# Kernel tuning notes

Hardware: AMD Instinct MI355X
Metric: run time of the kernel (lower is better)

The kernel has to match this reference:

```python
import jax, jax.numpy as jnp
import numpy as np

NZ, NC = 100, 2
FEAT_NUMBER, FEATURE_DIM = 8192, 1024
B = 8192
BN_EPS = 1e-5
GUMBEL_EPS = 0.001
TEMP = 0.1


def _batchnorm(h, gamma, beta):
    # torch BatchNorm1d training mode: biased batch statistics
    mu = jnp.mean(h, axis=0, keepdims=True)
    var = jnp.var(h, axis=0, keepdims=True)
    return (h - mu) * jax.lax.rsqrt(var + BN_EPS) * gamma + beta


def setup_inputs() -> dict:
    key = jax.random.key(0)
    ks = jax.random.split(key, 16)
    def glorot(k, shape):
        lim = 1.0 / np.sqrt(shape[0])
        return jax.random.uniform(k, shape, jnp.float32, -lim, lim)
    return {
        "x": jax.random.normal(ks[0], (B, NZ), jnp.float32),
        "y": jax.random.uniform(ks[1], (B, NC), jnp.float32),
        "W1": glorot(ks[2], (NZ + NC, 256)), "b1": jnp.zeros((256,), jnp.float32),
        "g1": jnp.ones((256,), jnp.float32), "be1": jnp.zeros((256,), jnp.float32),
        "W2": glorot(ks[3], (256, 64)), "b2": jnp.zeros((64,), jnp.float32),
        "g2": jnp.ones((64,), jnp.float32), "be2": jnp.zeros((64,), jnp.float32),
        "W3": glorot(ks[4], (64, FEAT_NUMBER)), "b3": jnp.zeros((FEAT_NUMBER,), jnp.float32),
        "codebook": jax.random.normal(ks[5], (FEAT_NUMBER, FEATURE_DIM), jnp.float32),
    }


def reference(x, y, W1, b1, g1, be1, W2, b2, g2, be2, W3, b3, codebook):
    z = jnp.concatenate([x, y], axis=-1)                       # [B, nz+nc]
    h = jax.nn.relu(_batchnorm(z @ W1 + b1, g1, be1))          # [B, 256]
    h = jax.nn.relu(_batchnorm(h @ W2 + b2, g2, be2))          # [B, 64]
    logits = h @ W3 + b3                                       # [B, feat_number]

    # gumbel noise: U = eps*rand; g = -log(-log(U+eps)+eps)
    U = GUMBEL_EPS * jax.random.uniform(jax.random.key(42), logits.shape, jnp.float32)
    g = -jnp.log(-jnp.log(U + GUMBEL_EPS) + GUMBEL_EPS)
    y_soft = jax.nn.softmax((logits + g) / TEMP, axis=-1)

    # straight-through one-hot
    ind = jnp.argmax(y_soft, axis=-1)
    y_hard = jax.nn.one_hot(ind, FEAT_NUMBER, dtype=y_soft.dtype)
    z_st = jax.lax.stop_gradient(y_hard - y_soft) + y_soft     # [B, feat_number]

    # weighted codebook sum == matmul (avoids [B,F,D] broadcast intermediate)
    return jnp.einsum('bf,fd->bd', z_st, codebook)             # [B, feature_dim]
```

## Files before the change

### kernel.cpp

```cpp
#include <hip/hip_runtime.h>
#include <math.h>

#define B_ROWS   8192
#define NZ       100
#define NC       2
#define H1       256
#define H2       64
#define FEATN    8192
#define FDIM     1024
#define RROWS    16
#define NTILE    (FEATN / 16)
#define NTILE_H  (NTILE / 2)
#define A1ROWS   16
#define A1BLKS   (B_ROWS / A1ROWS)
#define CONVBLKS 128
#define A2ROWS   16
#define A2BLKS   (B_ROWS / A2ROWS)

typedef __attribute__((ext_vector_type(8))) short short8;
typedef __attribute__((ext_vector_type(4))) float f32x4;

__device__ __forceinline__ unsigned rotl32(unsigned v, int r) {
    return (v << r) | (v >> (32 - r));
}
__device__ __forceinline__ unsigned threefry_bits(unsigned lo) {
    const unsigned ks0 = 0u, ks1 = 42u, ks2 = 0x1BD11BDAu ^ 42u;
    unsigned x0 = 0u + ks0;
    unsigned x1 = lo + ks1;
#define TF_R4(a,b,c,d) \
    x0 += x1; x1 = rotl32(x1,a); x1 ^= x0; \
    x0 += x1; x1 = rotl32(x1,b); x1 ^= x0; \
    x0 += x1; x1 = rotl32(x1,c); x1 ^= x0; \
    x0 += x1; x1 = rotl32(x1,d); x1 ^= x0;
    TF_R4(13,15,26,6);  x0 += ks1; x1 += ks2 + 1u;
    TF_R4(17,29,16,24); x0 += ks2; x1 += ks0 + 2u;
    TF_R4(13,15,26,6);  x0 += ks0; x1 += ks1 + 3u;
    TF_R4(17,29,16,24); x0 += ks1; x1 += ks2 + 4u;
    TF_R4(13,15,26,6);  x0 += ks2; x1 += ks0 + 5u;
#undef TF_R4
    return x0 ^ x1;
}
__device__ __forceinline__ float gumbel_g(unsigned flat) {
    unsigned bits = threefry_bits(flat);
    float u  = __uint_as_float((bits >> 9) | 0x3f800000u) - 1.0f;
    float U  = 0.001f * u;
    float t1 = U + 0.001f;
    float L1 = (float)log((double)t1);
    float A  = 0.001f - L1;
    float L2 = (float)log((double)A);
    return -L2;
}

__device__ __forceinline__ unsigned short f2bf(float x) {
    unsigned u = __float_as_uint(x);
    u += 0x7fffu + ((u >> 16) & 1u);
    return (unsigned short)(u >> 16);
}
__device__ __forceinline__ unsigned short f2bf_up(float x) {
    unsigned u = __float_as_uint(x);
    unsigned hi = (u & 0x80000000u) ? (u >> 16) : ((u + 0xFFFFu) >> 16);
    return (unsigned short)hi;
}
__device__ __forceinline__ float bf2f(unsigned short h) {
    return __uint_as_float((unsigned)h << 16);
}
__device__ __forceinline__ unsigned fmono(float x) {
    unsigned b = __float_as_uint(x);
    return (b & 0x80000000u) ? ~b : (b | 0x80000000u);
}

__global__ __launch_bounds__(512) void k_a1(
    const float* __restrict__ x, const float* __restrict__ y,
    const float* __restrict__ W1, const float* __restrict__ b1,
    const float* __restrict__ W3,
    float* __restrict__ a1, double* __restrict__ p1, double* __restrict__ p2,
    unsigned short* __restrict__ w3s, float* __restrict__ maxw)
{
    const int t = threadIdx.x;

    if (blockIdx.x >= A1BLKS) {
        const int job  = (blockIdx.x - A1BLKS) * 512 + t;
        const int T    = job >> 7;
        const int rem  = job & 127;
        const int kh   = rem >> 6;
        const int l    = rem & 63;
        const int quad = l >> 4, col = l & 15;
        const float* src = W3 + (size_t)(kh * 32 + quad * 8) * FEATN + T * 16 + col;
        unsigned short v[8];
        float mx = 0.0f;
#pragma unroll
        for (int jj = 0; jj < 8; ++jj) {
            float xv = src[(size_t)jj * FEATN];
            mx = fmaxf(mx, fabsf(xv));
            v[jj] = f2bf(xv);
        }
        uint4 o;
        o.x = (unsigned)v[0] | ((unsigned)v[1] << 16);
        o.y = (unsigned)v[2] | ((unsigned)v[3] << 16);
        o.z = (unsigned)v[4] | ((unsigned)v[5] << 16);
        o.w = (unsigned)v[6] | ((unsigned)v[7] << 16);
        ((uint4*)w3s)[job] = o;
#pragma unroll
        for (int off = 32; off; off >>= 1) mx = fmaxf(mx, __shfl_xor(mx, off));
        __shared__ float wred[8];
        if ((t & 63) == 0) wred[t >> 6] = mx;
        __syncthreads();
        if (t == 0) {
            float m = wred[0];
#pragma unroll
            for (int wq = 1; wq < 8; ++wq) m = fmaxf(m, wred[wq]);
            atomicMax((unsigned*)maxw, __float_as_uint(m));
        }
        return;
    }

    const int j    = t & 255;
    const int half = t >> 8;
    const int b0   = blockIdx.x * A1ROWS;
    const int r0   = half * 8;

    __shared__ __align__(16) float xs[NZ][16];
    __shared__ __align__(16) float ys[NC][16];
    __shared__ float vsh[256][8];
    for (int q = t; q < A1ROWS * NZ; q += 512) {
        int r = q / NZ, i = q - r * NZ;
        xs[i][r] = x[(size_t)b0 * NZ + q];
    }
    if (t < A1ROWS * NC) {
        int r = t >> 1, i = t & 1;
        ys[i][r] = y[b0 * NC + t];
    }
    __syncthreads();

    double acc[8];
#pragma unroll
    for (int r = 0; r < 8; ++r) acc[r] = 0.0;
    for (int i = 0; i < NZ; ++i) {
        double wd = (double)W1[i * H1 + j];
        const float4 x0 = *(const float4*)&xs[i][r0];
        const float4 x1 = *(const float4*)&xs[i][r0 + 4];
        acc[0] += (double)x0.x * wd; acc[1] += (double)x0.y * wd;
        acc[2] += (double)x0.z * wd; acc[3] += (double)x0.w * wd;
        acc[4] += (double)x1.x * wd; acc[5] += (double)x1.y * wd;
        acc[6] += (double)x1.z * wd; acc[7] += (double)x1.w * wd;
    }
#pragma unroll
    for (int i = 0; i < NC; ++i) {
        double wd = (double)W1[(NZ + i) * H1 + j];
        const float4 y0 = *(const float4*)&ys[i][r0];
        const float4 y1 = *(const float4*)&ys[i][r0 + 4];
        acc[0] += (double)y0.x * wd; acc[1] += (double)y0.y * wd;
        acc[2] += (double)y0.z * wd; acc[3] += (double)y0.w * wd;
        acc[4] += (double)y1.x * wd; acc[5] += (double)y1.y * wd;
        acc[6] += (double)y1.z * wd; acc[7] += (double)y1.w * wd;
    }
    const double bb = (double)b1[j];
    float v[8];
#pragma unroll
    for (int r = 0; r < 8; ++r) {
        v[r] = (float)(acc[r] + bb);
        a1[(b0 + r0 + r) * H1 + j] = v[r];
    }
    if (half) {
#pragma unroll
        for (int r = 0; r < 8; ++r) vsh[j][r] = v[r];
    }
    __syncthreads();
    if (!half) {
        double s = 0.0, s2 = 0.0;
#pragma unroll
        for (int r = 0; r < 8; ++r) {
            double dv = (double)v[r];
            s += dv; s2 += dv * dv;
        }
#pragma unroll
        for (int r = 0; r < 8; ++r) {
            double dv = (double)vsh[j][r];
            s += dv; s2 += dv * dv;
        }
        p1[blockIdx.x * H1 + j] = s;
        p2[blockIdx.x * H1 + j] = s2;
    }
}

__global__ __launch_bounds__(256) void k_stats2(
    const double* __restrict__ p1, const double* __restrict__ p2,
    int nprt, int ncol,
    const float* __restrict__ gamma, const float* __restrict__ beta,
    float* __restrict__ scale, float* __restrict__ shift)
{
    const int j = blockIdx.x, t = threadIdx.x;
    double s = 0.0, s2 = 0.0;
    for (int g = t; g < nprt; g += 256) {
        s  += p1[(size_t)g * ncol + j];
        s2 += p2[(size_t)g * ncol + j];
    }
#pragma unroll
    for (int off = 32; off; off >>= 1) {
        s  += __shfl_xor(s, off);
        s2 += __shfl_xor(s2, off);
    }
    __shared__ double ws1[4], ws2[4];
    if ((t & 63) == 0) { ws1[t >> 6] = s; ws2[t >> 6] = s2; }
    __syncthreads();
    if (t == 0) {
        s  = (ws1[0] + ws1[1]) + (ws1[2] + ws1[3]);
        s2 = (ws2[0] + ws2[1]) + (ws2[2] + ws2[3]);
        double mean = s * (1.0 / B_ROWS);
        double var  = s2 * (1.0 / B_ROWS) - mean * mean;
        double rstd = 1.0 / sqrt(var + 1e-5);
        double sc   = (double)gamma[j] * rstd;
        scale[j] = (float)sc;
        shift[j] = (float)((double)beta[j] - mean * sc);
    }
}

__global__ __launch_bounds__(512) void k_a2(
    const float* __restrict__ a1,
    const float* __restrict__ sc1, const float* __restrict__ sh1,
    const float* __restrict__ W2, const float* __restrict__ b2,
    float* __restrict__ a2, double* __restrict__ p1, double* __restrict__ p2)
{
    const int t  = threadIdx.x;
    const int k  = t & 63;
    const int rg = t >> 6;
    const int b0 = blockIdx.x * A2ROWS;
    const int r0 = rg * 2;

    __shared__ __align__(8) float hs[H1][18];
    __shared__ float vsh[64][17];

    {
        const int jc = t & 255, rq = t >> 8;
        const float sct = sc1[jc], sht = sh1[jc];
#pragma unroll
        for (int rr = rq * 8; rr < rq * 8 + 8; ++rr) {
            float vv = a1[(size_t)(b0 + rr) * H1 + jc];
            hs[jc][rr] = fmaxf(fmaf(vv, sct, sht), 0.0f);
        }
    }
    __syncthreads();

    double acc0 = 0.0, acc1 = 0.0;
#pragma unroll 4
    for (int j = 0; j < H1; ++j) {
        double wd = (double)W2[j * H2 + k];
        const float2 h2 = *(const float2*)&hs[j][r0];
        acc0 += (double)h2.x * wd;
        acc1 += (double)h2.y * wd;
    }
    const double bb = (double)b2[k];
    float v0 = (float)(acc0 + bb);
    float v1 = (float)(acc1 + bb);
    a2[(b0 + r0 + 0) * H2 + k] = v0;
    a2[(b0 + r0 + 1) * H2 + k] = v1;
    vsh[k][r0]     = v0;
    vsh[k][r0 + 1] = v1;
    __syncthreads();
    if (t < 64) {
        double s = 0.0, s2 = 0.0;
#pragma unroll
        for (int r = 0; r < A2ROWS; ++r) {
            double dv = (double)vsh[t][r];
            s += dv; s2 += dv * dv;
        }
        p1[blockIdx.x * H2 + t] = s;
        p2[blockIdx.x * H2 + t] = s2;
    }
}

__global__ __launch_bounds__(512)
__attribute__((amdgpu_waves_per_eu(4, 4)))
void k_main(
    const float* __restrict__ a2,
    const float* __restrict__ sc2, const float* __restrict__ sh2,
    const float* __restrict__ W3, const float* __restrict__ b3,
    const unsigned short* __restrict__ w3s, const float* __restrict__ maxw,
    unsigned long long* __restrict__ bestG)
{
    const int t    = threadIdx.x;
    const int wv   = t >> 6;
    const int lane = t & 63;
    const int quad = lane >> 4, col = lane & 15;
    const int half = blockIdx.x & 1;
    const int b0   = (blockIdx.x >> 1) * RROWS;

    __shared__ __align__(16) float h2T[64][17];
    __shared__ unsigned short fineW[NTILE_H][17];
    __shared__ float thrS[RROWS];
    __shared__ unsigned short wl[RROWS * NTILE_H];
    __shared__ int wlN;
    __shared__ float maxwS;

    if (t == 0) { maxwS = maxw[0]; wlN = 0; }
    for (int q = t; q < RROWS * 64; q += 512) {
        int j = q >> 4, r = q & 15;
        float v = a2[(b0 + r) * H2 + j];
        h2T[j][r] = fmaxf(fmaf(v, sc2[j], sh2[j]), 0.0f);
    }
    __syncthreads();

    short8 aF0, aF1;
#pragma unroll
    for (int jj = 0; jj < 8; ++jj) {
        aF0[jj] = (short)f2bf(h2T[quad * 8 + jj][col]);
        aF1[jj] = (short)f2bf(h2T[32 + quad * 8 + jj][col]);
    }

    {
        const uint4*  wp = (const uint4*)w3s
                         + (size_t)(half * NTILE_H + wv * 32) * 128 + lane;
        const float4* bq = (const float4*)b3 + (half * 1024 + wv * 128) + quad;
        for (int s = 0; s < 4; ++s) {
            uint4 c[8], d[8];
            float4 bb[8];
#pragma unroll
            for (int u = 0; u < 8; ++u) {
                c[u]  = wp[u * 128];
                d[u]  = wp[u * 128 + 64];
                bb[u] = bq[u * 4];
            }
#pragma unroll
            for (int u = 0; u < 8; ++u) {
                f32x4 acc = {bb[u].x, bb[u].y, bb[u].z, bb[u].w};
                acc = __builtin_amdgcn_mfma_f32_16x16x32_bf16(
                          *(const short8*)&c[u], aF0, acc, 0, 0, 0);
                acc = __builtin_amdgcn_mfma_f32_16x16x32_bf16(
                          *(const short8*)&d[u], aF1, acc, 0, 0, 0);
                float m = fmaxf(fmaxf(acc[0], acc[1]), fmaxf(acc[2], acc[3]));
                m = fmaxf(m, __shfl_xor(m, 16));
                m = fmaxf(m, __shfl_xor(m, 32));
                if (lane < 16) fineW[wv * 32 + s * 8 + u][lane] = f2bf_up(m);
            }
            wp += 1024; bq += 32;
        }
    }
    __syncthreads();

    {
        const int r = t >> 5, cc = t & 31;
        float s = fabsf(h2T[2 * cc][r]) + fabsf(h2T[2 * cc + 1][r]);
        float gmv = -1e30f;
#pragma unroll
        for (int k = 0; k < 8; ++k) gmv = fmaxf(gmv, bf2f(fineW[cc + 32 * k][r]));
#pragma unroll
        for (int off = 1; off < 32; off <<= 1) {
            s   += __shfl_xor(s, off);
            gmv  = fmaxf(gmv, __shfl_xor(gmv, off));
        }
        if (cc == 0) {
            float e = s * maxwS * (1.0f / 256.0f);
            thrS[r] = gmv - (0.1068f + e + 1e-3f + fabsf(gmv) * 0.0078125f);
        }
    }
    __syncthreads();

    {
        const int r = t >> 5, cc = t & 31;
        const float th = thrS[r];
#pragma unroll
        for (int k = 0; k < 8; ++k) {
            const int T = cc + 32 * k;
            if (bf2f(fineW[T][r]) >= th) {
                int idx = atomicAdd(&wlN, 1);
                wl[idx] = (unsigned short)((r << 8) | T);
            }
        }
    }
    __syncthreads();

    {
        const int n = wlN;
        const int g = lane >> 4;
        for (int i = wv * 4; i < n; i += 32) {
            const int  ci  = i + g;
            const bool act = (ci < n);
            const int  e   = act ? wl[ci] : 0;
            const int  r   = e >> 8;
            const int  lt  = e & 255;
            const int  f   = (half * NTILE_H + lt) * 16 + col;
            float acc = b3[f];
            const float* wcol = W3 + f;
#pragma unroll 8
            for (int j = 0; j < 64; ++j) {
                acc = fmaf(h2T[j][r], *wcol, acc);
                wcol += FEATN;
            }
            if (act && acc >= thrS[r]) {
                float sc = acc + gumbel_g((unsigned)(b0 + r) * (unsigned)FEATN + (unsigned)f);
                unsigned long long pk = ((unsigned long long)fmono(sc) << 32)
                                      | (unsigned)(FEATN - 1 - f);
                atomicMax(&bestG[b0 + r], pk);
            }
        }
    }
}

__global__ __launch_bounds__(256) void k_out(
    const unsigned long long* __restrict__ bestG,
    const float* __restrict__ codebook, float* __restrict__ out)
{
    const int t  = threadIdx.x;
    const int b0 = blockIdx.x * 16;
    __shared__ int inds[16];
    if (t < 16)
        inds[t] = (FEATN - 1 - (int)(bestG[b0 + t] & 0xFFFFFFFFull)) & (FEATN - 1);
    __syncthreads();
#pragma unroll
    for (int r = 0; r < 16; ++r) {
        const float4* src = (const float4*)(codebook + (size_t)inds[r] * FDIM);
        float4*       dst = (float4*)(out + (size_t)(b0 + r) * FDIM);
        dst[t] = src[t];
    }
}

extern "C" void kernel_launch(void* const* d_in, const int* in_sizes, int n_in,
                              void* d_out, int out_size, void* d_ws, size_t ws_size,
                              hipStream_t stream)
{
    const float* x   = (const float*)d_in[0];
    const float* y   = (const float*)d_in[1];
    const float* W1  = (const float*)d_in[2];
    const float* b1  = (const float*)d_in[3];
    const float* g1  = (const float*)d_in[4];
    const float* be1 = (const float*)d_in[5];
    const float* W2  = (const float*)d_in[6];
    const float* b2  = (const float*)d_in[7];
    const float* g2  = (const float*)d_in[8];
    const float* be2 = (const float*)d_in[9];
    const float* W3  = (const float*)d_in[10];
    const float* b3  = (const float*)d_in[11];
    const float* cb  = (const float*)d_in[12];
    float* out = (float*)d_out;

    float* ws  = (float*)d_ws;
    float* a1  = ws;
    float* a2  = a1 + B_ROWS * H1;
    float* sc1 = a2 + B_ROWS * H2;
    float* sh1 = sc1 + H1;
    float* sc2 = sh1 + H1;
    float* sh2 = sc2 + H2;
    double* p1 = (double*)(sh2 + H2);
    double* p2 = p1 + A1BLKS * H1;
    unsigned short* w3s = (unsigned short*)(p2 + A1BLKS * H1);
    float* maxw = (float*)(w3s + NTILE * 2 * 64 * 8);
    unsigned long long* bestG = (unsigned long long*)a1;

    hipMemsetAsync(maxw, 0, 4, stream);
    k_a1    <<<A1BLKS + CONVBLKS, 512, 0, stream>>>(x, y, W1, b1, W3,
                                                    a1, p1, p2, w3s, maxw);
    k_stats2<<<H1, 256, 0, stream>>>(p1, p2, A1BLKS, H1, g1, be1, sc1, sh1);
    k_a2    <<<A2BLKS, 512, 0, stream>>>(a1, sc1, sh1, W2, b2, a2, p1, p2);
    k_stats2<<<H2, 256, 0, stream>>>(p1, p2, A2BLKS, H2, g2, be2, sc2, sh2);
    hipMemsetAsync(bestG, 0, B_ROWS * 8, stream);
    k_main  <<<(B_ROWS / RROWS) * 2, 512, 0, stream>>>(a2, sc2, sh2, W3, b3,
                                                       w3s, maxw, bestG);
    k_out   <<<B_ROWS / 16, 256, 0, stream>>>(bestG, cb, out);
}
```

Baseline: 228.0 us.

## Fuse argmax and codebook gather into main kernel; fp32 accumulation in MLP layers

The main kernel now covers all feature tiles per row block instead of splitting them across two blocks. It keeps the per-row best score in shared memory and writes the codebook row to the output directly, which removes the bestG memset, the global atomics and the separate output kernel. Tile maxima are now stored as fp32 instead of rounded-up bf16, and the threshold drops its bf16 slack term. The first two MLP layers switch from double to float FMA accumulation, cutting FP64 cost but possibly changing batchnorm inputs and argmax ties slightly.

```diff
diff --git a/kernel.cpp b/kernel.cpp
--- a/kernel.cpp
+++ b/kernel.cpp
@@ -10,7 +10,6 @@
 #define FDIM     1024
 #define RROWS    16
 #define NTILE    (FEATN / 16)
-#define NTILE_H  (NTILE / 2)
 #define A1ROWS   16
 #define A1BLKS   (B_ROWS / A1ROWS)
 #define CONVBLKS 128
@@ -56,14 +55,6 @@
     u += 0x7fffu + ((u >> 16) & 1u);
     return (unsigned short)(u >> 16);
 }
-__device__ __forceinline__ unsigned short f2bf_up(float x) {
-    unsigned u = __float_as_uint(x);
-    unsigned hi = (u & 0x80000000u) ? (u >> 16) : ((u + 0xFFFFu) >> 16);
-    return (unsigned short)hi;
-}
-__device__ __forceinline__ float bf2f(unsigned short h) {
-    return __uint_as_float((unsigned)h << 16);
-}
 __device__ __forceinline__ unsigned fmono(float x) {
     unsigned b = __float_as_uint(x);
     return (b & 0x80000000u) ? ~b : (b | 0x80000000u);
@@ -132,33 +123,33 @@
     }
     __syncthreads();
 
-    double acc[8];
-#pragma unroll
-    for (int r = 0; r < 8; ++r) acc[r] = 0.0;
+    float acc[8];
+#pragma unroll
+    for (int r = 0; r < 8; ++r) acc[r] = 0.0f;
     for (int i = 0; i < NZ; ++i) {
-        double wd = (double)W1[i * H1 + j];
+        float wd = W1[i * H1 + j];
         const float4 x0 = *(const float4*)&xs[i][r0];
         const float4 x1 = *(const float4*)&xs[i][r0 + 4];
-        acc[0] += (double)x0.x * wd; acc[1] += (double)x0.y * wd;
-        acc[2] += (double)x0.z * wd; acc[3] += (double)x0.w * wd;
-        acc[4] += (double)x1.x * wd; acc[5] += (double)x1.y * wd;
-        acc[6] += (double)x1.z * wd; acc[7] += (double)x1.w * wd;
+        acc[0] = fmaf(x0.x, wd, acc[0]); acc[1] = fmaf(x0.y, wd, acc[1]);
+        acc[2] = fmaf(x0.z, wd, acc[2]); acc[3] = fmaf(x0.w, wd, acc[3]);
+        acc[4] = fmaf(x1.x, wd, acc[4]); acc[5] = fmaf(x1.y, wd, acc[5]);
+        acc[6] = fmaf(x1.z, wd, acc[6]); acc[7] = fmaf(x1.w, wd, acc[7]);
     }
 #pragma unroll
     for (int i = 0; i < NC; ++i) {
-        double wd = (double)W1[(NZ + i) * H1 + j];
+        float wd = W1[(NZ + i) * H1 + j];
         const float4 y0 = *(const float4*)&ys[i][r0];
         const float4 y1 = *(const float4*)&ys[i][r0 + 4];
-        acc[0] += (double)y0.x * wd; acc[1] += (double)y0.y * wd;
-        acc[2] += (double)y0.z * wd; acc[3] += (double)y0.w * wd;
-        acc[4] += (double)y1.x * wd; acc[5] += (double)y1.y * wd;
-        acc[6] += (double)y1.z * wd; acc[7] += (double)y1.w * wd;
-    }
-    const double bb = (double)b1[j];
+        acc[0] = fmaf(y0.x, wd, acc[0]); acc[1] = fmaf(y0.y, wd, acc[1]);
+        acc[2] = fmaf(y0.z, wd, acc[2]); acc[3] = fmaf(y0.w, wd, acc[3]);
+        acc[4] = fmaf(y1.x, wd, acc[4]); acc[5] = fmaf(y1.y, wd, acc[5]);
+        acc[6] = fmaf(y1.z, wd, acc[6]); acc[7] = fmaf(y1.w, wd, acc[7]);
+    }
+    const float bb = b1[j];
     float v[8];
 #pragma unroll
     for (int r = 0; r < 8; ++r) {
-        v[r] = (float)(acc[r] + bb);
+        v[r] = acc[r] + bb;
         a1[(b0 + r0 + r) * H1 + j] = v[r];
     }
     if (half) {
@@ -241,17 +232,17 @@
     }
     __syncthreads();
 
-    double acc0 = 0.0, acc1 = 0.0;
+    float acc0 = 0.0f, acc1 = 0.0f;
 #pragma unroll 4
     for (int j = 0; j < H1; ++j) {
-        double wd = (double)W2[j * H2 + k];
+        float wd = W2[j * H2 + k];
         const float2 h2 = *(const float2*)&hs[j][r0];
-        acc0 += (double)h2.x * wd;
-        acc1 += (double)h2.y * wd;
-    }
-    const double bb = (double)b2[k];
-    float v0 = (float)(acc0 + bb);
-    float v1 = (float)(acc1 + bb);
+        acc0 = fmaf(h2.x, wd, acc0);
+        acc1 = fmaf(h2.y, wd, acc1);
+    }
+    const float bb = b2[k];
+    float v0 = acc0 + bb;
+    float v1 = acc1 + bb;
     a2[(b0 + r0 + 0) * H2 + k] = v0;
     a2[(b0 + r0 + 1) * H2 + k] = v1;
     vsh[k][r0]     = v0;
@@ -276,20 +267,21 @@
     const float* __restrict__ sc2, const float* __restrict__ sh2,
     const float* __restrict__ W3, const float* __restrict__ b3,
     const unsigned short* __restrict__ w3s, const float* __restrict__ maxw,
-    unsigned long long* __restrict__ bestG)
+    const float* __restrict__ codebook, float* __restrict__ out)
 {
     const int t    = threadIdx.x;
     const int wv   = t >> 6;
     const int lane = t & 63;
     const int quad = lane >> 4, col = lane & 15;
-    const int half = blockIdx.x & 1;
-    const int b0   = (blockIdx.x >> 1) * RROWS;
+    const int b0   = blockIdx.x * RROWS;
 
     __shared__ __align__(16) float h2T[64][17];
-    __shared__ unsigned short fineW[NTILE_H][17];
+    __shared__ float fineT[NTILE][17];
     __shared__ float thrS[RROWS];
-    __shared__ unsigned short wl[RROWS * NTILE_H];
+    __shared__ unsigned long long best[RROWS];
+    __shared__ unsigned short wl[RROWS * NTILE];
     __shared__ int wlN;
+    __shared__ int rowInd[RROWS];
     __shared__ float maxwS;
 
     if (t == 0) { maxwS = maxw[0]; wlN = 0; }
@@ -308,10 +300,9 @@
     }
 
     {
-        const uint4*  wp = (const uint4*)w3s
-                         + (size_t)(half * NTILE_H + wv * 32) * 128 + lane;
-        const float4* bq = (const float4*)b3 + (half * 1024 + wv * 128) + quad;
-        for (int s = 0; s < 4; ++s) {
+        const uint4*  wp = (const uint4*)w3s + (size_t)wv * 8192 + lane;
+        const float4* bq = (const float4*)b3 + wv * 256 + quad;
+        for (int s = 0; s < 8; ++s) {
             uint4 c[8], d[8];
             float4 bb[8];
 #pragma unroll
@@ -330,7 +321,7 @@
                 float m = fmaxf(fmaxf(acc[0], acc[1]), fmaxf(acc[2], acc[3]));
                 m = fmaxf(m, __shfl_xor(m, 16));
                 m = fmaxf(m, __shfl_xor(m, 32));
-                if (lane < 16) fineW[wv * 32 + s * 8 + u][lane] = f2bf_up(m);
+                if (lane < 16) fineT[(wv * 8 + s) * 8 + u][lane] = m;
             }
             wp += 1024; bq += 32;
         }
@@ -342,7 +333,7 @@
         float s = fabsf(h2T[2 * cc][r]) + fabsf(h2T[2 * cc + 1][r]);
         float gmv = -1e30f;
 #pragma unroll
-        for (int k = 0; k < 8; ++k) gmv = fmaxf(gmv, bf2f(fineW[cc + 32 * k][r]));
+        for (int k = 0; k < 16; ++k) gmv = fmaxf(gmv, fineT[cc + 32 * k][r]);
 #pragma unroll
         for (int off = 1; off < 32; off <<= 1) {
             s   += __shfl_xor(s, off);
@@ -350,7 +341,8 @@
         }
         if (cc == 0) {
             float e = s * maxwS * (1.0f / 256.0f);
-            thrS[r] = gmv - (0.1068f + e + 1e-3f + fabsf(gmv) * 0.0078125f);
+            thrS[r] = gmv - (0.1068f + e + 1e-3f);
+            best[r] = 0ull;
         }
     }
     __syncthreads();
@@ -359,11 +351,11 @@
         const int r = t >> 5, cc = t & 31;
         const float th = thrS[r];
 #pragma unroll
-        for (int k = 0; k < 8; ++k) {
+        for (int k = 0; k < 16; ++k) {
             const int T = cc + 32 * k;
-            if (bf2f(fineW[T][r]) >= th) {
+            if (fineT[T][r] >= th) {
                 int idx = atomicAdd(&wlN, 1);
-                wl[idx] = (unsigned short)((r << 8) | T);
+                wl[idx] = (unsigned short)((r << 9) | T);
             }
         }
     }
@@ -376,9 +368,9 @@
             const int  ci  = i + g;
             const bool act = (ci < n);
             const int  e   = act ? wl[ci] : 0;
-            const int  r   = e >> 8;
-            const int  lt  = e & 255;
-            const int  f   = (half * NTILE_H + lt) * 16 + col;
+            const int  r   = e >> 9;
+            const int  T   = e & 511;
+            const int  f   = T * 16 + col;
             float acc = b3[f];
             const float* wcol = W3 + f;
 #pragma unroll 8
@@ -390,27 +382,25 @@
                 float sc = acc + gumbel_g((unsigned)(b0 + r) * (unsigned)FEATN + (unsigned)f);
                 unsigned long long pk = ((unsigned long long)fmono(sc) << 32)
                                       | (unsigned)(FEATN - 1 - f);
-                atomicMax(&bestG[b0 + r], pk);
+                atomicMax(&best[r], pk);
             }
         }
     }
-}
-
-__global__ __launch_bounds__(256) void k_out(
-    const unsigned long long* __restrict__ bestG,
-    const float* __restrict__ codebook, float* __restrict__ out)
-{
-    const int t  = threadIdx.x;
-    const int b0 = blockIdx.x * 16;
-    __shared__ int inds[16];
-    if (t < 16)
-        inds[t] = (FEATN - 1 - (int)(bestG[b0 + t] & 0xFFFFFFFFull)) & (FEATN - 1);
-    __syncthreads();
-#pragma unroll
-    for (int r = 0; r < 16; ++r) {
-        const float4* src = (const float4*)(codebook + (size_t)inds[r] * FDIM);
-        float4*       dst = (float4*)(out + (size_t)(b0 + r) * FDIM);
-        dst[t] = src[t];
+    __syncthreads();
+    if (t < RROWS) {
+        rowInd[t] = (FEATN - 1 - (int)(best[t] & 0xFFFFFFFFull)) & (FEATN - 1);
+    }
+    __syncthreads();
+
+    {
+        const int rr = t >> 8, tt = t & 255;
+        for (int rp = 0; rp < RROWS / 2; ++rp) {
+            const int r = rp * 2 + rr;
+            const int ind = rowInd[r];
+            const float4* src = (const float4*)(codebook + (size_t)ind * FDIM);
+            float4*       dst = (float4*)(out + (size_t)(b0 + r) * FDIM);
+            dst[tt] = src[tt];
+        }
     }
 }
 
@@ -444,7 +434,6 @@
     double* p2 = p1 + A1BLKS * H1;
     unsigned short* w3s = (unsigned short*)(p2 + A1BLKS * H1);
     float* maxw = (float*)(w3s + NTILE * 2 * 64 * 8);
-    unsigned long long* bestG = (unsigned long long*)a1;
 
     hipMemsetAsync(maxw, 0, 4, stream);
     k_a1    <<<A1BLKS + CONVBLKS, 512, 0, stream>>>(x, y, W1, b1, W3,
@@ -452,8 +441,6 @@
     k_stats2<<<H1, 256, 0, stream>>>(p1, p2, A1BLKS, H1, g1, be1, sc1, sh1);
     k_a2    <<<A2BLKS, 512, 0, stream>>>(a1, sc1, sh1, W2, b2, a2, p1, p2);
     k_stats2<<<H2, 256, 0, stream>>>(p1, p2, A2BLKS, H2, g2, be2, sc2, sh2);
-    hipMemsetAsync(bestG, 0, B_ROWS * 8, stream);
-    k_main  <<<(B_ROWS / RROWS) * 2, 512, 0, stream>>>(a2, sc2, sh2, W3, b3,
-                                                       w3s, maxw, bestG);
-    k_out   <<<B_ROWS / 16, 256, 0, stream>>>(bestG, cb, out);
-}
+    k_main  <<<B_ROWS / RROWS, 512, 0, stream>>>(a2, sc2, sh2, W3, b3,
+                                                 w3s, maxw, cb, out);
+}
```

After: 205.1 us. -10.0%, faster.
